# Kernel optimization log

Measured on AMD Instinct MI355X. Metric: run time of the kernel, lower is better.

## Reference

```python
import jax, jax.numpy as jnp
import numpy as np

B, S, V, H, NL, NH = 16, 512, 512, 1024, 8, 16
DH = H // NH
F = 4 * H
NEG = jnp.float32(-1e9)


def setup_inputs() -> dict:
    key = jax.random.key(0)
    ks = jax.random.split(key, 8)
    s = 0.02
    return {
        'input_ids': jax.random.randint(ks[0], (B, S), 0, V, dtype=jnp.int32),
        'split_positions': jax.random.randint(ks[1], (B,), 1, S, dtype=jnp.int32),
        'emb': jax.random.normal(ks[2], (V, H), jnp.float32) * s,
        'ln1_g': jnp.ones((NL, H), jnp.float32),
        'ln1_b': jnp.zeros((NL, H), jnp.float32),
        'Wqkv': jax.random.normal(ks[3], (NL, H, 3 * H), jnp.float32) * s,
        'bqkv': jnp.zeros((NL, 3 * H), jnp.float32),
        'Wo': jax.random.normal(ks[4], (NL, H, H), jnp.float32) * s,
        'bo': jnp.zeros((NL, H), jnp.float32),
        'ln2_g': jnp.ones((NL, H), jnp.float32),
        'ln2_b': jnp.zeros((NL, H), jnp.float32),
        'Wfc': jax.random.normal(ks[5], (NL, H, F), jnp.float32) * s,
        'bfc': jnp.zeros((NL, F), jnp.float32),
        'Wproj': jax.random.normal(ks[6], (NL, F, H), jnp.float32) * s,
        'bproj': jnp.zeros((NL, H), jnp.float32),
        'lnf_g': jnp.ones((H,), jnp.float32),
        'lnf_b': jnp.zeros((H,), jnp.float32),
    }


def _ln(x, g, b):
    mu = x.mean(-1, keepdims=True)
    var = ((x - mu) ** 2).mean(-1, keepdims=True)
    return (x - mu) * jax.lax.rsqrt(var + 1e-5) * g + b


def _alibi_slopes(n):
    # standard ALiBi geometric slopes for power-of-2 head counts
    return jnp.asarray(2.0 ** (-8.0 * np.arange(1, n + 1) / n), jnp.float32)


def reference(input_ids, split_positions, emb, ln1_g, ln1_b, Wqkv, bqkv, Wo, bo,
              ln2_g, ln2_b, Wfc, bfc, Wproj, bproj, lnf_g, lnf_b):
    Bq, L = input_ids.shape
    i = jnp.arange(L)[:, None]
    j = jnp.arange(L)[None, :]
    causal = j <= i  # [L,L] True = attend allowed
    sp = split_positions[:, None, None]
    # tokens at/after split may NOT attend to tokens before split
    blocked = (i[None] >= sp) & (j[None] < sp)  # [B,L,L]
    allowed = causal[None] & ~blocked  # [B,L,L]
    slopes = _alibi_slopes(NH)
    alibi = -slopes[:, None, None] * (i - j).astype(jnp.float32)  # [NH,L,L]
    bias = jnp.where(allowed[:, None], alibi[None], NEG)  # [B,NH,L,L]

    x = emb[input_ids]  # [B,L,H]
    scale = 1.0 / np.sqrt(DH)
    for l in range(NL):
        h = _ln(x, ln1_g[l], ln1_b[l])
        qkv = h @ Wqkv[l] + bqkv[l]
        q, k, v = [t.reshape(Bq, L, NH, DH) for t in jnp.split(qkv, 3, axis=-1)]
        sc = jnp.einsum('bind,bjnd->bnij', q, k) * scale + bias
        p = jax.nn.softmax(sc, axis=-1)
        a = jnp.einsum('bnij,bjnd->bind', p, v).reshape(Bq, L, H)
        x = x + a @ Wo[l] + bo[l]
        h = _ln(x, ln2_g[l], ln2_b[l])
        x = x + jax.nn.gelu(h @ Wfc[l] + bfc[l], approximate=True) @ Wproj[l] + bproj[l]
    x = _ln(x, lnf_g, lnf_b)
    return x @ emb.T  # tied lm_head
```

## Files before the change

kernel.cpp:

```cpp
#include <hip/hip_runtime.h>
#include <hip/hip_bf16.h>

#define B_  16
#define S_  512
#define V_  512
#define H_  1024
#define NL_ 8
#define NH_ 16
#define DH_ 64
#define F_  4096

typedef __attribute__((ext_vector_type(8))) short bf16x8;
typedef __attribute__((ext_vector_type(4))) float f32x4;

__device__ __forceinline__ float gelu_tanh(float x) {
  float x3 = x * x * x;
  return 0.5f * x * (1.0f + tanhf(0.7978845608028654f * (x + 0.044715f * x3)));
}

__device__ __forceinline__ void gload_lds16(const void* g, void* l) {
  __builtin_amdgcn_global_load_lds(
      (const __attribute__((address_space(1))) unsigned int*)(unsigned long long)g,
      (__attribute__((address_space(3))) unsigned int*)(unsigned long long)l,
      16, 0, 0);
}

__global__ __launch_bounds__(256) void transpose_cvt(const float* __restrict__ W,
                                                     __hip_bfloat16* __restrict__ WT,
                                                     int K, int N) {
  __shared__ float tile[32][33];
  int l = blockIdx.z;
  int k0 = blockIdx.y * 32, n0 = blockIdx.x * 32;
  const float* Wl = W + (size_t)l * K * N;
  __hip_bfloat16* WTl = WT + (size_t)l * N * K;
  int tx = threadIdx.x, ty = threadIdx.y;
  #pragma unroll
  for (int i = 0; i < 32; i += 8)
    tile[ty + i][tx] = Wl[(size_t)(k0 + ty + i) * N + n0 + tx];
  __syncthreads();
  #pragma unroll
  for (int i = 0; i < 32; i += 8)
    WTl[(size_t)(n0 + ty + i) * K + k0 + tx] = __float2bfloat16(tile[tx][ty + i]);
}

__global__ __launch_bounds__(256) void cvt_bf16(const float* __restrict__ in,
                                                __hip_bfloat16* __restrict__ out) {
  int i = (blockIdx.x * 256 + threadIdx.x) * 4;
  float4 v = *(const float4*)(in + i);
  out[i + 0] = __float2bfloat16(v.x);
  out[i + 1] = __float2bfloat16(v.y);
  out[i + 2] = __float2bfloat16(v.z);
  out[i + 3] = __float2bfloat16(v.w);
}

__global__ __launch_bounds__(256) void embed_k(const int* __restrict__ ids,
                                               const float* __restrict__ emb,
                                               float* __restrict__ x) {
  int t = blockIdx.x;
  int v = ids[t];
  int d = threadIdx.x * 4;
  float4 val = *(const float4*)(emb + (size_t)v * H_ + d);
  *(float4*)(x + (size_t)t * H_ + d) = val;
}

__global__ __launch_bounds__(256) void ln_k(const float* __restrict__ x,
                                            const float* __restrict__ g,
                                            const float* __restrict__ b,
                                            __hip_bfloat16* __restrict__ out) {
  int t = blockIdx.x;
  const float* xr = x + (size_t)t * H_;
  float4 v = ((const float4*)xr)[threadIdx.x];
  float s = v.x + v.y + v.z + v.w;
  float q = v.x * v.x + v.y * v.y + v.z * v.z + v.w * v.w;
  #pragma unroll
  for (int off = 32; off; off >>= 1) {
    s += __shfl_down(s, off);
    q += __shfl_down(q, off);
  }
  __shared__ float ps[4], pq[4];
  __shared__ float mu_s, rstd_s;
  int wave = threadIdx.x >> 6, lane = threadIdx.x & 63;
  if (lane == 0) { ps[wave] = s; pq[wave] = q; }
  __syncthreads();
  if (threadIdx.x == 0) {
    float S = ps[0] + ps[1] + ps[2] + ps[3];
    float Q = pq[0] + pq[1] + pq[2] + pq[3];
    float mu = S * (1.0f / H_);
    float var = Q * (1.0f / H_) - mu * mu;
    mu_s = mu;
    rstd_s = rsqrtf(var + 1e-5f);
  }
  __syncthreads();
  float mu = mu_s, rstd = rstd_s;
  int d = threadIdx.x * 4;
  float4 gv = ((const float4*)g)[threadIdx.x];
  float4 bv = ((const float4*)b)[threadIdx.x];
  __hip_bfloat16* op = out + (size_t)t * H_ + d;
  op[0] = __float2bfloat16((v.x - mu) * rstd * gv.x + bv.x);
  op[1] = __float2bfloat16((v.y - mu) * rstd * gv.y + bv.y);
  op[2] = __float2bfloat16((v.z - mu) * rstd * gv.z + bv.z);
  op[3] = __float2bfloat16((v.w - mu) * rstd * gv.w + bv.w);
}

template <int MODE>
__global__ __launch_bounds__(256) void gemm_bt(const __hip_bfloat16* __restrict__ A,
                                               const __hip_bfloat16* __restrict__ BT,
                                               const float* __restrict__ bias,
                                               void* __restrict__ Cv,
                                               int M, int N, int K) {
  constexpr int BM = 128, BN = 128, BK = 32;
  __shared__ __hip_bfloat16 As[BM * BK];
  __shared__ __hip_bfloat16 Bs[BN * BK];
  const int tid = threadIdx.x;
  const int m0 = blockIdx.y * BM, n0 = blockIdx.x * BN;
  const int wave = tid >> 6, lane = tid & 63;
  const int wr = (wave >> 1) * 64, wc = (wave & 1) * 64;
  const int quad = lane >> 4, l16 = lane & 15;

  f32x4 acc[4][4];
  #pragma unroll
  for (int i = 0; i < 4; i++)
    #pragma unroll
    for (int j = 0; j < 4; j++) acc[i][j] = (f32x4){0.f, 0.f, 0.f, 0.f};

  const int srow = (lane >> 2), scol = (lane & 3) * 8;
  const __hip_bfloat16* agp0 = A + (size_t)(m0 + wave * 32 + srow) * K + scol;
  const __hip_bfloat16* agp1 = agp0 + (size_t)16 * K;
  const __hip_bfloat16* bgp0 = BT + (size_t)(n0 + wave * 32 + srow) * K + scol;
  const __hip_bfloat16* bgp1 = bgp0 + (size_t)16 * K;
  __hip_bfloat16* al0 = As + (wave * 32) * 32;
  __hip_bfloat16* al1 = As + (wave * 32 + 16) * 32;
  __hip_bfloat16* bl0 = Bs + (wave * 32) * 32;
  __hip_bfloat16* bl1 = Bs + (wave * 32 + 16) * 32;

  for (int k0 = 0; k0 < K; k0 += BK) {
    __syncthreads();
    gload_lds16(agp0, al0);
    gload_lds16(agp1, al1);
    gload_lds16(bgp0, bl0);
    gload_lds16(bgp1, bl1);
    agp0 += BK; agp1 += BK; bgp0 += BK; bgp1 += BK;
    __syncthreads();
    bf16x8 af[4], bfr[4];
    #pragma unroll
    for (int mt = 0; mt < 4; mt++)
      af[mt] = *(const bf16x8*)(&As[(wr + mt * 16 + l16) * 32 + quad * 8]);
    #pragma unroll
    for (int nt = 0; nt < 4; nt++)
      bfr[nt] = *(const bf16x8*)(&Bs[(wc + nt * 16 + l16) * 32 + quad * 8]);
    #pragma unroll
    for (int mt = 0; mt < 4; mt++)
      #pragma unroll
      for (int nt = 0; nt < 4; nt++)
        acc[mt][nt] = __builtin_amdgcn_mfma_f32_16x16x32_bf16(af[mt], bfr[nt], acc[mt][nt], 0, 0, 0);
  }

  #pragma unroll
  for (int mt = 0; mt < 4; mt++) {
    #pragma unroll
    for (int nt = 0; nt < 4; nt++) {
      int col = n0 + wc + nt * 16 + l16;
      float bv = bias ? bias[col] : 0.f;
      #pragma unroll
      for (int rr = 0; rr < 4; rr++) {
        int row = m0 + wr + mt * 16 + quad * 4 + rr;
        float v = acc[mt][nt][rr] + bv;
        if constexpr (MODE == 0) {
          ((__hip_bfloat16*)Cv)[(size_t)row * N + col] = __float2bfloat16(v);
        } else if constexpr (MODE == 1) {
          ((__hip_bfloat16*)Cv)[(size_t)row * N + col] = __float2bfloat16(gelu_tanh(v));
        } else if constexpr (MODE == 2) {
          ((float*)Cv)[(size_t)row * N + col] = v;
        } else {
          ((float*)Cv)[(size_t)row * N + col] += v;
        }
      }
    }
  }
}

__global__ __launch_bounds__(256) void attn_mfma(const __hip_bfloat16* __restrict__ qkv,
                                                 const int* __restrict__ split_positions,
                                                 __hip_bfloat16* __restrict__ out) {
  constexpr int LD = 66;
  __shared__ __hip_bfloat16 Qs[64 * LD];
  __shared__ __hip_bfloat16 Ks[64 * LD];
  __shared__ __hip_bfloat16 Vt[64 * LD];
  __shared__ __hip_bfloat16 Ps[64 * LD];

  const int bid = blockIdx.x;
  const int qt = bid & 7;
  const int hh = (bid >> 3) & 15;
  const int b = bid >> 7;
  const int sp = split_positions[b];
  const int i0 = qt * 64;
  const int tid = threadIdx.x;
  const int wave = tid >> 6, lane = tid & 63;
  const int quad = lane >> 4, l16 = lane & 15;
  const float slope = exp2f(-0.5f * (float)(hh + 1));
  const size_t rs = 3 * H_;
  const size_t base = (size_t)b * S_ * rs + (size_t)hh * DH_;

  {
    int r = tid >> 2, d = (tid & 3) * 16;
    const __hip_bfloat16* qp = qkv + base + (size_t)(i0 + r) * rs + d;
    uint4 u0 = *(const uint4*)qp;
    uint4 u1 = *(const uint4*)(qp + 8);
    *(uint4*)&Qs[r * LD + d] = u0;
    *(uint4*)&Qs[r * LD + d + 8] = u1;
  }

  float m_i[4], l_i[4];
  f32x4 acc_o[4];
  #pragma unroll
  for (int rr = 0; rr < 4; rr++) { m_i[rr] = -INFINITY; l_i[rr] = 0.f; }
  #pragma unroll
  for (int nt = 0; nt < 4; nt++) acc_o[nt] = (f32x4){0.f, 0.f, 0.f, 0.f};

  const int i_row_base = i0 + wave * 16 + quad * 4;
  const int ktiles = qt + 1;

  for (int kt = 0; kt < ktiles; kt++) {
    const int j0 = kt * 64;
    __syncthreads();
    {
      int r = tid >> 2, d = (tid & 3) * 16;
      const __hip_bfloat16* kp = qkv + base + H_ + (size_t)(j0 + r) * rs + d;
      uint4 k0v = *(const uint4*)kp;
      uint4 k1v = *(const uint4*)(kp + 8);
      *(uint4*)&Ks[r * LD + d] = k0v;
      *(uint4*)&Ks[r * LD + d + 8] = k1v;
      const __hip_bfloat16* vp = kp + H_;
      uint4 v0 = *(const uint4*)vp;
      uint4 v1 = *(const uint4*)(vp + 8);
      const __hip_bfloat16* vv0 = (const __hip_bfloat16*)&v0;
      const __hip_bfloat16* vv1 = (const __hip_bfloat16*)&v1;
      #pragma unroll
      for (int i = 0; i < 8; i++) Vt[(d + i) * LD + r] = vv0[i];
      #pragma unroll
      for (int i = 0; i < 8; i++) Vt[(d + 8 + i) * LD + r] = vv1[i];
    }
    __syncthreads();

    f32x4 acc_s[4];
    #pragma unroll
    for (int nt = 0; nt < 4; nt++) acc_s[nt] = (f32x4){0.f, 0.f, 0.f, 0.f};
    bf16x8 aq0 = *(const bf16x8*)&Qs[(wave * 16 + l16) * LD + quad * 8];
    bf16x8 aq1 = *(const bf16x8*)&Qs[(wave * 16 + l16) * LD + 32 + quad * 8];
    #pragma unroll
    for (int nt = 0; nt < 4; nt++) {
      bf16x8 bk0 = *(const bf16x8*)&Ks[(nt * 16 + l16) * LD + quad * 8];
      bf16x8 bk1 = *(const bf16x8*)&Ks[(nt * 16 + l16) * LD + 32 + quad * 8];
      acc_s[nt] = __builtin_amdgcn_mfma_f32_16x16x32_bf16(aq0, bk0, acc_s[nt], 0, 0, 0);
      acc_s[nt] = __builtin_amdgcn_mfma_f32_16x16x32_bf16(aq1, bk1, acc_s[nt], 0, 0, 0);
    }

    float tm[4] = {-INFINITY, -INFINITY, -INFINITY, -INFINITY};
    #pragma unroll
    for (int nt = 0; nt < 4; nt++) {
      int j = j0 + nt * 16 + l16;
      #pragma unroll
      for (int rr = 0; rr < 4; rr++) {
        int i_row = i_row_base + rr;
        float s = acc_s[nt][rr] * 0.125f + slope * (float)(j - i_row);
        bool masked = (j > i_row) || (i_row >= sp && j < sp);
        s = masked ? -1e9f : s;
        acc_s[nt][rr] = s;
        tm[rr] = fmaxf(tm[rr], s);
      }
    }
    #pragma unroll
    for (int rr = 0; rr < 4; rr++) {
      #pragma unroll
      for (int off = 1; off < 16; off <<= 1) tm[rr] = fmaxf(tm[rr], __shfl_xor(tm[rr], off));
    }

    float alpha[4], psum[4];
    #pragma unroll
    for (int rr = 0; rr < 4; rr++) {
      float mn = fmaxf(m_i[rr], tm[rr]);
      alpha[rr] = __expf(m_i[rr] - mn);
      m_i[rr] = mn;
      psum[rr] = 0.f;
    }
    #pragma unroll
    for (int nt = 0; nt < 4; nt++) {
      #pragma unroll
      for (int rr = 0; rr < 4; rr++) {
        float p = __expf(acc_s[nt][rr] - m_i[rr]);
        acc_s[nt][rr] = p;
        psum[rr] += p;
      }
    }
    #pragma unroll
    for (int rr = 0; rr < 4; rr++) {
      #pragma unroll
      for (int off = 1; off < 16; off <<= 1) psum[rr] += __shfl_xor(psum[rr], off);
      l_i[rr] = l_i[rr] * alpha[rr] + psum[rr];
    }

    #pragma unroll
    for (int nt = 0; nt < 4; nt++)
      #pragma unroll
      for (int rr = 0; rr < 4; rr++)
        Ps[(wave * 16 + quad * 4 + rr) * LD + nt * 16 + l16] = __float2bfloat16(acc_s[nt][rr]);

    #pragma unroll
    for (int nt = 0; nt < 4; nt++) {
      #pragma unroll
      for (int rr = 0; rr < 4; rr++) acc_o[nt][rr] *= alpha[rr];
    }
    bf16x8 ap0 = *(const bf16x8*)&Ps[(wave * 16 + l16) * LD + quad * 8];
    bf16x8 ap1 = *(const bf16x8*)&Ps[(wave * 16 + l16) * LD + 32 + quad * 8];
    #pragma unroll
    for (int nt = 0; nt < 4; nt++) {
      bf16x8 bv0 = *(const bf16x8*)&Vt[(nt * 16 + l16) * LD + quad * 8];
      bf16x8 bv1 = *(const bf16x8*)&Vt[(nt * 16 + l16) * LD + 32 + quad * 8];
      acc_o[nt] = __builtin_amdgcn_mfma_f32_16x16x32_bf16(ap0, bv0, acc_o[nt], 0, 0, 0);
      acc_o[nt] = __builtin_amdgcn_mfma_f32_16x16x32_bf16(ap1, bv1, acc_o[nt], 0, 0, 0);
    }
  }

  float inv[4];
  #pragma unroll
  for (int rr = 0; rr < 4; rr++) inv[rr] = 1.0f / l_i[rr];
  #pragma unroll
  for (int nt = 0; nt < 4; nt++) {
    #pragma unroll
    for (int rr = 0; rr < 4; rr++) {
      size_t row = (size_t)b * S_ + i_row_base + rr;
      out[row * H_ + hh * DH_ + nt * 16 + l16] = __float2bfloat16(acc_o[nt][rr] * inv[rr]);
    }
  }
}

extern "C" void kernel_launch(void* const* d_in, const int* in_sizes, int n_in,
                              void* d_out, int out_size, void* d_ws, size_t ws_size,
                              hipStream_t stream) {
  const int* ids = (const int*)d_in[0];
  const int* sp = (const int*)d_in[1];
  const float* emb = (const float*)d_in[2];
  const float* ln1_g = (const float*)d_in[3];
  const float* ln1_b = (const float*)d_in[4];
  const float* Wqkv = (const float*)d_in[5];
  const float* bqkv = (const float*)d_in[6];
  const float* Wo = (const float*)d_in[7];
  const float* bo = (const float*)d_in[8];
  const float* ln2_g = (const float*)d_in[9];
  const float* ln2_b = (const float*)d_in[10];
  const float* Wfc = (const float*)d_in[11];
  const float* bfc = (const float*)d_in[12];
  const float* Wproj = (const float*)d_in[13];
  const float* bproj = (const float*)d_in[14];
  const float* lnf_g = (const float*)d_in[15];
  const float* lnf_b = (const float*)d_in[16];

  char* p = (char*)d_ws;
  __hip_bfloat16* WqkvT = (__hip_bfloat16*)p; p += (size_t)NL_ * 3 * H_ * H_ * 2;
  __hip_bfloat16* WoT = (__hip_bfloat16*)p;   p += (size_t)NL_ * H_ * H_ * 2;
  __hip_bfloat16* WfcT = (__hip_bfloat16*)p;  p += (size_t)NL_ * F_ * H_ * 2;
  __hip_bfloat16* WprojT = (__hip_bfloat16*)p; p += (size_t)NL_ * H_ * F_ * 2;
  __hip_bfloat16* embb = (__hip_bfloat16*)p;  p += (size_t)V_ * H_ * 2;
  float* x = (float*)p;                        p += (size_t)B_ * S_ * H_ * 4;
  __hip_bfloat16* h = (__hip_bfloat16*)p;     p += (size_t)B_ * S_ * H_ * 2;
  __hip_bfloat16* qkv = (__hip_bfloat16*)p;   p += (size_t)B_ * S_ * 3 * H_ * 2;
  __hip_bfloat16* g = (__hip_bfloat16*)p;     p += (size_t)B_ * S_ * F_ * 2;

  dim3 tb(32, 8);
  transpose_cvt<<<dim3(3 * H_ / 32, H_ / 32, NL_), tb, 0, stream>>>(Wqkv, WqkvT, H_, 3 * H_);
  transpose_cvt<<<dim3(H_ / 32, H_ / 32, NL_), tb, 0, stream>>>(Wo, WoT, H_, H_);
  transpose_cvt<<<dim3(F_ / 32, H_ / 32, NL_), tb, 0, stream>>>(Wfc, WfcT, H_, F_);
  transpose_cvt<<<dim3(H_ / 32, F_ / 32, NL_), tb, 0, stream>>>(Wproj, WprojT, F_, H_);
  cvt_bf16<<<V_ * H_ / 1024, 256, 0, stream>>>(emb, embb);
  embed_k<<<B_ * S_, 256, 0, stream>>>(ids, emb, x);

  const int M = B_ * S_;
  for (int l = 0; l < NL_; l++) {
    ln_k<<<M, 256, 0, stream>>>(x, ln1_g + l * H_, ln1_b + l * H_, h);
    gemm_bt<0><<<dim3(3 * H_ / 128, M / 128), 256, 0, stream>>>(
        h, WqkvT + (size_t)l * 3 * H_ * H_, bqkv + l * 3 * H_, qkv, M, 3 * H_, H_);
    attn_mfma<<<B_ * NH_ * (S_ / 64), 256, 0, stream>>>(qkv, sp, h);
    gemm_bt<3><<<dim3(H_ / 128, M / 128), 256, 0, stream>>>(
        h, WoT + (size_t)l * H_ * H_, bo + l * H_, x, M, H_, H_);
    ln_k<<<M, 256, 0, stream>>>(x, ln2_g + l * H_, ln2_b + l * H_, h);
    gemm_bt<1><<<dim3(F_ / 128, M / 128), 256, 0, stream>>>(
        h, WfcT + (size_t)l * F_ * H_, bfc + l * F_, g, M, F_, H_);
    gemm_bt<3><<<dim3(H_ / 128, M / 128), 256, 0, stream>>>(
        g, WprojT + (size_t)l * H_ * F_, bproj + l * H_, x, M, H_, F_);
  }
  ln_k<<<M, 256, 0, stream>>>(x, lnf_g, lnf_b, h);
  gemm_bt<2><<<dim3(V_ / 128, M / 128), 256, 0, stream>>>(h, embb, nullptr, d_out, M, V_, H_);
}
```

Baseline: 4.251 ms.

## Double-buffer GEMM LDS tiles, swizzle blocks per XCD, shrink M tile for N=1024 GEMMs

New measurement: 3.983 ms. -6.3%, faster.

```diff
diff --git a/kernel.cpp b/kernel.cpp
--- a/kernel.cpp
+++ b/kernel.cpp
@@ -102,61 +102,77 @@
   op[3] = __float2bfloat16((v.w - mu) * rstd * gv.w + bv.w);
 }
 
-template <int MODE>
+template <int MODE, int MT>
 __global__ __launch_bounds__(256) void gemm_bt(const __hip_bfloat16* __restrict__ A,
                                                const __hip_bfloat16* __restrict__ BT,
                                                const float* __restrict__ bias,
                                                void* __restrict__ Cv,
                                                int M, int N, int K) {
-  constexpr int BM = 128, BN = 128, BK = 32;
-  __shared__ __hip_bfloat16 As[BM * BK];
-  __shared__ __hip_bfloat16 Bs[BN * BK];
+  constexpr int BM = MT * 32, BN = 128, BK = 32;
+  constexpr int ACALLS = MT / 2;
+  __shared__ __hip_bfloat16 As[2][BM * BK];
+  __shared__ __hip_bfloat16 Bs[2][BN * BK];
   const int tid = threadIdx.x;
-  const int m0 = blockIdx.y * BM, n0 = blockIdx.x * BN;
   const int wave = tid >> 6, lane = tid & 63;
-  const int wr = (wave >> 1) * 64, wc = (wave & 1) * 64;
   const int quad = lane >> 4, l16 = lane & 15;
-
-  f32x4 acc[4][4];
-  #pragma unroll
-  for (int i = 0; i < 4; i++)
+  const int wr = (wave >> 1) * 16 * MT, wc = (wave & 1) * 64;
+
+  const int nbn = N / BN;
+  int bid = blockIdx.x, m_blk, n_blk;
+  if ((nbn & 7) == 0) {
+    const int g = nbn >> 3;
+    const int xcd = bid & 7, local = bid >> 3;
+    n_blk = xcd * g + local % g;
+    m_blk = local / g;
+  } else {
+    n_blk = bid % nbn;
+    m_blk = bid / nbn;
+  }
+  const int m0 = m_blk * BM, n0 = n_blk * BN;
+
+  f32x4 acc[MT][4];
+  #pragma unroll
+  for (int i = 0; i < MT; i++)
     #pragma unroll
     for (int j = 0; j < 4; j++) acc[i][j] = (f32x4){0.f, 0.f, 0.f, 0.f};
 
-  const int srow = (lane >> 2), scol = (lane & 3) * 8;
-  const __hip_bfloat16* agp0 = A + (size_t)(m0 + wave * 32 + srow) * K + scol;
-  const __hip_bfloat16* agp1 = agp0 + (size_t)16 * K;
-  const __hip_bfloat16* bgp0 = BT + (size_t)(n0 + wave * 32 + srow) * K + scol;
-  const __hip_bfloat16* bgp1 = bgp0 + (size_t)16 * K;
-  __hip_bfloat16* al0 = As + (wave * 32) * 32;
-  __hip_bfloat16* al1 = As + (wave * 32 + 16) * 32;
-  __hip_bfloat16* bl0 = Bs + (wave * 32) * 32;
-  __hip_bfloat16* bl1 = Bs + (wave * 32 + 16) * 32;
-
+  const int srow = lane >> 2, scol = (lane & 3) * 8;
+  const __hip_bfloat16* agp = A + (size_t)(m0 + wave * 16 * ACALLS + srow) * K + scol;
+  const __hip_bfloat16* bgp = BT + (size_t)(n0 + wave * 32 + srow) * K + scol;
+  const int aoff = (wave * 16 * ACALLS) * 32;
+  const int boff = (wave * 32) * 32;
+
+  auto stage = [&](int buf, int kofs) {
+    #pragma unroll
+    for (int c = 0; c < ACALLS; c++)
+      gload_lds16(agp + (size_t)c * 16 * K + kofs, &As[buf][aoff + c * 512]);
+    #pragma unroll
+    for (int c = 0; c < 2; c++)
+      gload_lds16(bgp + (size_t)c * 16 * K + kofs, &Bs[buf][boff + c * 512]);
+  };
+
+  stage(0, 0);
+  int cur = 0;
   for (int k0 = 0; k0 < K; k0 += BK) {
     __syncthreads();
-    gload_lds16(agp0, al0);
-    gload_lds16(agp1, al1);
-    gload_lds16(bgp0, bl0);
-    gload_lds16(bgp1, bl1);
-    agp0 += BK; agp1 += BK; bgp0 += BK; bgp1 += BK;
-    __syncthreads();
-    bf16x8 af[4], bfr[4];
-    #pragma unroll
-    for (int mt = 0; mt < 4; mt++)
-      af[mt] = *(const bf16x8*)(&As[(wr + mt * 16 + l16) * 32 + quad * 8]);
+    if (k0 + BK < K) stage(cur ^ 1, k0 + BK);
+    bf16x8 af[MT], bfr[4];
+    #pragma unroll
+    for (int mt = 0; mt < MT; mt++)
+      af[mt] = *(const bf16x8*)(&As[cur][(wr + mt * 16 + l16) * 32 + quad * 8]);
     #pragma unroll
     for (int nt = 0; nt < 4; nt++)
-      bfr[nt] = *(const bf16x8*)(&Bs[(wc + nt * 16 + l16) * 32 + quad * 8]);
-    #pragma unroll
-    for (int mt = 0; mt < 4; mt++)
+      bfr[nt] = *(const bf16x8*)(&Bs[cur][(wc + nt * 16 + l16) * 32 + quad * 8]);
+    #pragma unroll
+    for (int mt = 0; mt < MT; mt++)
       #pragma unroll
       for (int nt = 0; nt < 4; nt++)
         acc[mt][nt] = __builtin_amdgcn_mfma_f32_16x16x32_bf16(af[mt], bfr[nt], acc[mt][nt], 0, 0, 0);
-  }
-
-  #pragma unroll
-  for (int mt = 0; mt < 4; mt++) {
+    cur ^= 1;
+  }
+
+  #pragma unroll
+  for (int mt = 0; mt < MT; mt++) {
     #pragma unroll
     for (int nt = 0; nt < 4; nt++) {
       int col = n0 + wc + nt * 16 + l16;
@@ -377,17 +393,17 @@
   const int M = B_ * S_;
   for (int l = 0; l < NL_; l++) {
     ln_k<<<M, 256, 0, stream>>>(x, ln1_g + l * H_, ln1_b + l * H_, h);
-    gemm_bt<0><<<dim3(3 * H_ / 128, M / 128), 256, 0, stream>>>(
+    gemm_bt<0, 4><<<(M / 128) * (3 * H_ / 128), 256, 0, stream>>>(
         h, WqkvT + (size_t)l * 3 * H_ * H_, bqkv + l * 3 * H_, qkv, M, 3 * H_, H_);
     attn_mfma<<<B_ * NH_ * (S_ / 64), 256, 0, stream>>>(qkv, sp, h);
-    gemm_bt<3><<<dim3(H_ / 128, M / 128), 256, 0, stream>>>(
+    gemm_bt<3, 2><<<(M / 64) * (H_ / 128), 256, 0, stream>>>(
         h, WoT + (size_t)l * H_ * H_, bo + l * H_, x, M, H_, H_);
     ln_k<<<M, 256, 0, stream>>>(x, ln2_g + l * H_, ln2_b + l * H_, h);
-    gemm_bt<1><<<dim3(F_ / 128, M / 128), 256, 0, stream>>>(
+    gemm_bt<1, 4><<<(M / 128) * (F_ / 128), 256, 0, stream>>>(
         h, WfcT + (size_t)l * F_ * H_, bfc + l * F_, g, M, F_, H_);
-    gemm_bt<3><<<dim3(H_ / 128, M / 128), 256, 0, stream>>>(
+    gemm_bt<3, 2><<<(M / 64) * (H_ / 128), 256, 0, stream>>>(
         g, WprojT + (size_t)l * H_ * F_, bproj + l * H_, x, M, H_, F_);
   }
   ln_k<<<M, 256, 0, stream>>>(x, lnf_g, lnf_b, h);
-  gemm_bt<2><<<dim3(V_ / 128, M / 128), 256, 0, stream>>>(h, embb, nullptr, d_out, M, V_, H_);
-}
+  gemm_bt<2, 4><<<(M / 128) * (V_ / 128), 256, 0, stream>>>(h, embb, nullptr, d_out, M, V_, H_);
+}
```
